# Kernel tuning notes

Measured on AMD Instinct MI355X. Metric: run time of the kernel, lower is better.

The kernel has to match this reference:

```python
import jax, jax.numpy as jnp
import numpy as np

N_PFAS, N_GW, N_SW = 20000, 100000, 20000
D_IN, D_OUT = 64, 128
E_PG, E_GP, E_SP, E_PS = 1600000, 1600000, 400000, 400000


def setup_inputs() -> dict:
    key = jax.random.key(0)
    ks = jax.random.split(key, 32)
    nrm = lambda k, shp, s=1.0: jax.random.normal(k, shp, jnp.float32) * s
    W = 0.05  # weight init scale
    inp = {
        # node features
        "x_pfas": nrm(ks[0], (N_PFAS, D_IN)),
        "x_gw": nrm(ks[1], (N_GW, D_IN)),
        "x_sw": nrm(ks[2], (N_SW, D_IN)),
        # edge indices per relation (src, dst)
        "ei_pg_src": jax.random.randint(ks[3], (E_PG,), 0, N_PFAS),
        "ei_pg_dst": jax.random.randint(ks[4], (E_PG,), 0, N_GW),
        "ei_gp_src": jax.random.randint(ks[5], (E_GP,), 0, N_GW),
        "ei_gp_dst": jax.random.randint(ks[6], (E_GP,), 0, N_PFAS),
        "ei_sp_src": jax.random.randint(ks[7], (E_SP,), 0, N_SW),
        "ei_sp_dst": jax.random.randint(ks[8], (E_SP,), 0, N_PFAS),
        "ei_ps_src": jax.random.randint(ks[9], (E_PS,), 0, N_PFAS),
        "ei_ps_dst": jax.random.randint(ks[10], (E_PS,), 0, N_SW),
        # SAGEConv params per relation: lin_l (neighbors, with bias), lin_r (root, no bias)
        "Wl_pg": nrm(ks[11], (D_IN, D_OUT), W), "Wr_pg": nrm(ks[12], (D_IN, D_OUT), W), "b_pg": jnp.zeros((D_OUT,), jnp.float32),
        "Wl_gp": nrm(ks[13], (D_IN, D_OUT), W), "Wr_gp": nrm(ks[14], (D_IN, D_OUT), W), "b_gp": jnp.zeros((D_OUT,), jnp.float32),
        "Wl_sp": nrm(ks[15], (D_IN, D_OUT), W), "Wr_sp": nrm(ks[16], (D_IN, D_OUT), W), "b_sp": jnp.zeros((D_OUT,), jnp.float32),
        "Wl_ps": nrm(ks[17], (D_IN, D_OUT), W), "Wr_ps": nrm(ks[18], (D_IN, D_OUT), W), "b_ps": jnp.zeros((D_OUT,), jnp.float32),
        # final linear head + PReLU
        "W_lin": nrm(ks[19], (D_OUT, 1), W), "b_lin": jnp.zeros((1,), jnp.float32),
        "alpha": jnp.full((1,), 0.25, jnp.float32),
    }
    return inp


def _sage(x_src, x_dst, src, dst, Wl, Wr, b, n_dst):
    # PyG SAGEConv: out = lin_l(mean_{j in N(i)} x_j) + lin_r(x_i)
    msg = x_src[src]                                   # [E, D_in] gather
    agg = jax.ops.segment_sum(msg, dst, num_segments=n_dst)        # [n_dst, D_in]
    cnt = jax.ops.segment_sum(jnp.ones(src.shape, x_src.dtype), dst, num_segments=n_dst)
    mean = agg / jnp.maximum(cnt, 1.0)[:, None]
    return mean @ Wl + x_dst @ Wr + b


def _prelu(y, a):
    return jnp.where(y > 0, y, a * y)


def reference(x_pfas, x_gw, x_sw, ei_pg_src, ei_pg_dst, ei_gp_src, ei_gp_dst,
              ei_sp_src, ei_sp_dst, ei_ps_src, ei_ps_dst,
              Wl_pg, Wr_pg, b_pg, Wl_gp, Wr_gp, b_gp, Wl_sp, Wr_sp, b_sp,
              Wl_ps, Wr_ps, b_ps, W_lin, b_lin, alpha):
    # HeteroConv with aggr='sum': pfas_sites receives from two relations (summed)
    h_gw = jax.nn.relu(_sage(x_pfas, x_gw, ei_pg_src, ei_pg_dst, Wl_pg, Wr_pg, b_pg, N_GW))
    h_pfas = jax.nn.relu(
        _sage(x_gw, x_pfas, ei_gp_src, ei_gp_dst, Wl_gp, Wr_gp, b_gp, N_PFAS)
        + _sage(x_sw, x_pfas, ei_sp_src, ei_sp_dst, Wl_sp, Wr_sp, b_sp, N_PFAS))
    h_sw = jax.nn.relu(_sage(x_pfas, x_sw, ei_ps_src, ei_ps_dst, Wl_ps, Wr_ps, b_ps, N_SW))
    out_gw = _prelu(h_gw @ W_lin + b_lin, alpha)   # [N_GW, 1]
    out_sw = _prelu(h_sw @ W_lin + b_lin, alpha)   # [N_SW, 1]
    return (h_pfas, out_gw, out_sw)
```

## Files before the change

kernel.cpp:

```cpp
#include <hip/hip_runtime.h>
#include <hip/hip_bf16.h>

#define N_PFAS 20000
#define N_GW   100000
#define N_SW   20000
#define N_SEG  160000
#define BASE_GW 0
#define BASE_GP 100000
#define BASE_SP 120000
#define BASE_PS 140000
#define NBIN 1250
#define NB_FILL 512
#define SORT_CAP 12288
#define N_XROW 140000

typedef __attribute__((ext_vector_type(8))) short short8;
typedef __attribute__((ext_vector_type(4))) float f32x4;
typedef __attribute__((ext_vector_type(2))) float f32x2;

__device__ __forceinline__ unsigned short f2bf(float f) {
    union { float f; unsigned int u; } v;
    v.f = f;
    unsigned int u = v.u;
    unsigned int r = (u + 0x7fffu + ((u >> 16) & 1u)) >> 16;
    return (unsigned short)r;
}
__device__ __forceinline__ float lo_bf(unsigned int v) {
    union { unsigned int u; float f; } w; w.u = v << 16; return w.f;
}
__device__ __forceinline__ float hi_bf(unsigned int v) {
    union { unsigned int u; float f; } w; w.u = v & 0xffff0000u; return w.f;
}

#if __has_builtin(__builtin_amdgcn_cvt_pk_f32_fp8) && __has_builtin(__builtin_amdgcn_cvt_pk_fp8_f32)
#define FP8_HW 1
__device__ __forceinline__ unsigned int enc_fp8x4(float4 v) {
    int r = __builtin_amdgcn_cvt_pk_fp8_f32(v.x, v.y, 0, false);
    r = __builtin_amdgcn_cvt_pk_fp8_f32(v.z, v.w, r, true);
    return (unsigned int)r;
}
__device__ __forceinline__ void dec_fp8x4v(unsigned int u, f32x2& lo, f32x2& hi) {
    lo = __builtin_amdgcn_cvt_pk_f32_fp8(u, false);
    hi = __builtin_amdgcn_cvt_pk_f32_fp8(u, true);
}
#else
__device__ __forceinline__ unsigned char enc1_e5m2(float f) {
    union { unsigned short u; _Float16 h; } cv;
    cv.h = (_Float16)f;
    unsigned int u = cv.u;
    unsigned int r = (u + 0x7Fu + ((u >> 8) & 1u)) >> 8;
    return (unsigned char)(r > 255u ? 255u : r);
}
__device__ __forceinline__ unsigned int enc_fp8x4(float4 v) {
    return (unsigned int)enc1_e5m2(v.x) | ((unsigned int)enc1_e5m2(v.y) << 8)
         | ((unsigned int)enc1_e5m2(v.z) << 16) | ((unsigned int)enc1_e5m2(v.w) << 24);
}
__device__ __forceinline__ float dec1_e5m2(unsigned int b) {
    union { unsigned short u; _Float16 h; } cv;
    cv.u = (unsigned short)(b << 8);
    return (float)cv.h;
}
__device__ __forceinline__ void dec_fp8x4v(unsigned int u, f32x2& lo, f32x2& hi) {
    lo.x = dec1_e5m2(u & 0xFF); lo.y = dec1_e5m2((u >> 8) & 0xFF);
    hi.x = dec1_e5m2((u >> 16) & 0xFF); hi.y = dec1_e5m2(u >> 24);
}
#endif

__device__ __forceinline__ void edge_lookup(int i,
    const int* __restrict__ s0, const int* __restrict__ d0, int E0,
    const int* __restrict__ s1, const int* __restrict__ d1, int E1,
    const int* __restrict__ s2, const int* __restrict__ d2, int E2,
    const int* __restrict__ s3, const int* __restrict__ d3,
    int& g, int& sv)
{
    if (i < E0)                { g = BASE_GW + d0[i];                 sv = s0[i]; }
    else if (i < E0 + E1)      { int j = i - E0;           g = BASE_GP + d1[j]; sv = s1[j]; }
    else if (i < E0 + E1 + E2) { int j = i - E0 - E1;      g = BASE_SP + d2[j]; sv = s2[j]; }
    else                       { int j = i - E0 - E1 - E2; g = BASE_PS + d3[j]; sv = s3[j]; }
}

__global__ void __launch_bounds__(1024)
count_cast(const int* __restrict__ d0, int E0, const int* __restrict__ d1, int E1,
           const int* __restrict__ d2, int E2, const int* __restrict__ d3, int E3,
           const float* __restrict__ xp, const float* __restrict__ xg,
           const float* __restrict__ xs, unsigned short* __restrict__ x16,
           unsigned int* __restrict__ x8, int* __restrict__ countMat)
{
    const int T0 = 20000 * 16, T1 = 120000 * 16, TT = N_XROW * 16;
    for (int i = blockIdx.x * 1024 + threadIdx.x; i < TT; i += NB_FILL * 1024) {
        float4 v;
        if (i < T0)      v = ((const float4*)xp)[i];
        else if (i < T1) v = ((const float4*)xg)[i - T0];
        else             v = ((const float4*)xs)[i - T1];
        ushort4 o;
        o.x = f2bf(v.x); o.y = f2bf(v.y); o.z = f2bf(v.z); o.w = f2bf(v.w);
        ((ushort4*)x16)[i] = o;
        if (x8) x8[i] = enc_fp8x4(v);
    }

    __shared__ int h[NBIN];
    for (int i = threadIdx.x; i < NBIN; i += 1024) h[i] = 0;
    __syncthreads();
    int total = E0 + E1 + E2 + E3;
    int CH = (total + NB_FILL - 1) / NB_FILL;
    int s = blockIdx.x * CH;
    int e = s + CH; if (e > total) e = total;
    for (int i0 = s + threadIdx.x * 4; i0 < e; i0 += 1024 * 4) {
        int gs[4];
        int m = e - i0; if (m > 4) m = 4;
        #pragma unroll
        for (int u = 0; u < 4; u++) {
            if (u < m) {
                int g, sv;
                edge_lookup(i0 + u, nullptr, d0, E0, nullptr, d1, E1,
                            nullptr, d2, E2, nullptr, d3, g, gs[u]);
                gs[u] = g;
            }
        }
        #pragma unroll
        for (int u = 0; u < 4; u++)
            if (u < m) atomicAdd(&h[gs[u] >> 7], 1);
    }
    __syncthreads();
    for (int i = threadIdx.x; i < NBIN; i += 1024)
        countMat[blockIdx.x * NBIN + i] = h[i];
}

__global__ void __launch_bounds__(1024)
scan_part(const int* __restrict__ countMat, int* __restrict__ next,
          int* __restrict__ partials, int n)
{
    __shared__ int lds[1024];
    int i = blockIdx.x * 1024 + threadIdx.x;
    int v = 0;
    if (i < n) {
        int b = i >> 9, k = i & 511;
        v = countMat[k * NBIN + b];
    }
    lds[threadIdx.x] = v;
    __syncthreads();
    #pragma unroll
    for (int off = 1; off < 1024; off <<= 1) {
        int t = (threadIdx.x >= off) ? lds[threadIdx.x - off] : 0;
        __syncthreads();
        lds[threadIdx.x] += t;
        __syncthreads();
    }
    if (i < n) next[i] = lds[threadIdx.x] - v;
    if (threadIdx.x == 1023) partials[blockIdx.x] = lds[1023];
}

__device__ __forceinline__ int partials_prefix(const int* __restrict__ partials,
                                               int idx, int lane)
{
    int s = 0;
    for (int j = lane; j < idx; j += 64) s += partials[j];
    #pragma unroll
    for (int m = 32; m; m >>= 1) s += __shfl_xor(s, m);
    return s;
}

__global__ void __launch_bounds__(1024)
fill_bin(const int* __restrict__ s0, const int* __restrict__ d0, int E0,
         const int* __restrict__ s1, const int* __restrict__ d1, int E1,
         const int* __restrict__ s2, const int* __restrict__ d2, int E2,
         const int* __restrict__ s3, const int* __restrict__ d3, int E3,
         const int* __restrict__ next, const int* __restrict__ partials,
         int* __restrict__ edge_binned)
{
    __shared__ int cur[NBIN];
    __shared__ int sp[1024];
    {
        int t = threadIdx.x;
        int v = (t < 625) ? partials[t] : 0;
        sp[t] = v;
        __syncthreads();
        #pragma unroll
        for (int off = 1; off < 1024; off <<= 1) {
            int x = (t >= off) ? sp[t - off] : 0;
            __syncthreads();
            sp[t] += x;
            __syncthreads();
        }
        sp[t] -= v;
    }
    __syncthreads();
    for (int i = threadIdx.x; i < NBIN; i += 1024)
        cur[i] = next[i * NB_FILL + blockIdx.x] + sp[i >> 1];
    __syncthreads();
    int total = E0 + E1 + E2 + E3;
    int CH = (total + NB_FILL - 1) / NB_FILL;
    int s = blockIdx.x * CH;
    int e = s + CH; if (e > total) e = total;
    for (int i0 = s + threadIdx.x * 4; i0 < e; i0 += 1024 * 4) {
        int g[4], sv[4];
        int m = e - i0; if (m > 4) m = 4;
        #pragma unroll
        for (int u = 0; u < 4; u++)
            if (u < m) edge_lookup(i0 + u, s0, d0, E0, s1, d1, E1,
                                   s2, d2, E2, s3, d3, g[u], sv[u]);
        #pragma unroll
        for (int u = 0; u < 4; u++) {
            if (u < m) {
                int slot = atomicAdd(&cur[g[u] >> 7], 1);
                edge_binned[slot] = sv[u] | ((g[u] & 127) << 20);
            }
        }
    }
}

__global__ void __launch_bounds__(1024)
sort_bin(const int* __restrict__ next, const int* __restrict__ partials,
         int* __restrict__ edge_binned,
         int2* __restrict__ nodeMeta, int E_total)
{
    __shared__ int stage[SORT_CAP];
    __shared__ int cnt[128], basep[128], cur[128];
    int lane = threadIdx.x & 63;
    int b = (int)((blockIdx.x + 781u) % NBIN);
    int pA = partials_prefix(partials, b >> 1, lane);
    int start = next[b * NB_FILL] + pA;
    int end;
    if (b == NBIN - 1) end = E_total;
    else {
        int pB = pA + ((b & 1) ? partials[b >> 1] : 0);
        end = next[(b + 1) * NB_FILL] + pB;
    }
    int n = end - start;
    if (n > SORT_CAP) n = SORT_CAP;

    for (int i = threadIdx.x; i < n; i += 1024) stage[i] = edge_binned[start + i];
    if (threadIdx.x < 128) cnt[threadIdx.x] = 0;
    __syncthreads();
    for (int i = threadIdx.x; i < n; i += 1024) atomicAdd(&cnt[stage[i] >> 20], 1);
    __syncthreads();
    if (threadIdx.x < 128) basep[threadIdx.x] = cnt[threadIdx.x];
    __syncthreads();
    #pragma unroll
    for (int off = 1; off < 128; off <<= 1) {
        int v = 0;
        if (threadIdx.x < 128 && threadIdx.x >= off) v = basep[threadIdx.x - off];
        __syncthreads();
        if (threadIdx.x < 128) basep[threadIdx.x] += v;
        __syncthreads();
    }
    if (threadIdx.x < 128) {
        int ex = basep[threadIdx.x] - cnt[threadIdx.x];
        cur[threadIdx.x] = ex;
        int g = (b << 7) + threadIdx.x;
        nodeMeta[g] = make_int2(start + ex, cnt[threadIdx.x]);
    }
    __syncthreads();
    for (int i = threadIdx.x; i < n; i += 1024) {
        int w = stage[i];
        int dl = w >> 20;
        int g = (b << 7) + dl;
        int rb = (g < BASE_GP) ? 0 : (g < BASE_SP) ? 20000
               : (g < BASE_PS) ? 120000 : 0;
        int slot = atomicAdd(&cur[dl], 1);
        edge_binned[start + slot] = (w & 0xFFFFF) + rb;
    }
}

__global__ void __launch_bounds__(256)
agg_node8(const unsigned int* __restrict__ x8,
          const int2* __restrict__ nodeMeta,
          const int* __restrict__ edge_src, unsigned short* __restrict__ meanAll)
{
    int wpair = (blockIdx.x * blockDim.x + threadIdx.x) >> 6;
    int lane = threadIdx.x & 63;
    if (wpair >= N_SEG / 2) return;
    int h = lane >> 5;
    int wlin = 2 * wpair + h;
    int wid = (wlin < 60000) ? (BASE_GP + wlin) : (wlin - 60000);
    int eq = (lane >> 3) & 3;
    int fc = lane & 7;
    int l32 = lane & 31;
    int2 meta = nodeMeta[wid];
    int start = meta.x, cnt = meta.y;
    f32x2 a01 = {0.f,0.f}, a23 = {0.f,0.f}, a45 = {0.f,0.f}, a67 = {0.f,0.f};
    int j = 0;
    for (; j + 32 <= cnt; j += 32) {
        int ev = edge_src[start + j + l32];
        #pragma unroll
        for (int t = 0; t < 8; t++) {
            int id = __shfl(ev, h * 32 + 4 * t + eq);
            uint2 v = *(const uint2*)(x8 + (((size_t)id) << 4) + fc * 2);
            f32x2 lo0, hi0, lo1, hi1;
            dec_fp8x4v(v.x, lo0, hi0);
            dec_fp8x4v(v.y, lo1, hi1);
            a01 += lo0; a23 += hi0; a45 += lo1; a67 += hi1;
        }
    }
    if (j < cnt) {
        int blk = cnt - j;
        int ev = (l32 < blk) ? edge_src[start + j + l32] : 0;
        int ng = (blk + 3) >> 2;
        for (int t = 0; t < ng; t++) {
            int idx = 4 * t + eq;
            int id = __shfl(ev, h * 32 + idx);
            if (idx < blk) {
                uint2 v = *(const uint2*)(x8 + (((size_t)id) << 4) + fc * 2);
                f32x2 lo0, hi0, lo1, hi1;
                dec_fp8x4v(v.x, lo0, hi0);
                dec_fp8x4v(v.y, lo1, hi1);
                a01 += lo0; a23 += hi0; a45 += lo1; a67 += hi1;
            }
        }
    }
    float f[8] = {a01.x, a01.y, a23.x, a23.y, a45.x, a45.y, a67.x, a67.y};
    #pragma unroll
    for (int r = 0; r < 8; r++) {
        f[r] += __shfl_xor(f[r], 8);
        f[r] += __shfl_xor(f[r], 16);
    }
    if (eq == 0) {
        float inv = 1.0f / (float)(cnt > 1 ? cnt : 1);
        ushort4 o0, o1;
        o0.x = f2bf(f[0] * inv); o0.y = f2bf(f[1] * inv);
        o0.z = f2bf(f[2] * inv); o0.w = f2bf(f[3] * inv);
        o1.x = f2bf(f[4] * inv); o1.y = f2bf(f[5] * inv);
        o1.z = f2bf(f[6] * inv); o1.w = f2bf(f[7] * inv);
        ushort4* dst = (ushort4*)(meanAll + (size_t)wid * 64 + fc * 8);
        dst[0] = o0;
        dst[1] = o1;
    }
}

__global__ void __launch_bounds__(256)
agg_node16(const unsigned short* __restrict__ x16,
           const int2* __restrict__ nodeMeta,
           const int* __restrict__ edge_src, unsigned short* __restrict__ meanAll)
{
    int wlin = (blockIdx.x * blockDim.x + threadIdx.x) >> 6;
    int lane = threadIdx.x & 63;
    if (wlin >= N_SEG) return;
    int wid = (wlin < 60000) ? (BASE_GP + wlin) : (wlin - 60000);
    int quarter = lane >> 4;
    int fcol = lane & 15;
    int2 meta = nodeMeta[wid];
    int start = meta.x, cnt = meta.y;
    float a0 = 0.f, a1 = 0.f, a2 = 0.f, a3 = 0.f;
    int j = 0;
    while (j + 64 <= cnt) {
        int ev = edge_src[start + j + lane];
        #pragma unroll
        for (int t = 0; t < 16; t++) {
            int id = __shfl(ev, 4 * t + quarter);
            uint2 v = ((const uint2*)(x16 + (((size_t)id) << 6)))[fcol];
            a0 += lo_bf(v.x); a1 += hi_bf(v.x);
            a2 += lo_bf(v.y); a3 += hi_bf(v.y);
        }
        j += 64;
    }
    if (j < cnt) {
        int blk = cnt - j;
        int ev = (lane < blk) ? edge_src[start + j + lane] : 0;
        int ng = (blk + 3) >> 2;
        #pragma unroll 4
        for (int t = 0; t < ng; t++) {
            int idx = 4 * t + quarter;
            int id = __shfl(ev, idx);
            if (idx < blk) {
                uint2 v = ((const uint2*)(x16 + (((size_t)id) << 6)))[fcol];
                a0 += lo_bf(v.x); a1 += hi_bf(v.x);
                a2 += lo_bf(v.y); a3 += hi_bf(v.y);
            }
        }
    }
    a0 += __shfl_xor(a0, 16); a1 += __shfl_xor(a1, 16);
    a2 += __shfl_xor(a2, 16); a3 += __shfl_xor(a3, 16);
    a0 += __shfl_xor(a0, 32); a1 += __shfl_xor(a1, 32);
    a2 += __shfl_xor(a2, 32); a3 += __shfl_xor(a3, 32);
    if (quarter == 0) {
        float inv = 1.0f / (float)(cnt > 1 ? cnt : 1);
        ushort4 o;
        o.x = f2bf(a0 * inv); o.y = f2bf(a1 * inv);
        o.z = f2bf(a2 * inv); o.w = f2bf(a3 * inv);
        ((ushort4*)meanAll)[(size_t)wid * 16 + fcol] = o;
    }
}

__device__ __forceinline__ void
head_body(const unsigned short* __restrict__ x16r,
          const unsigned short* __restrict__ mean,
          const float* __restrict__ Wl, const float* __restrict__ Wr,
          const float* __restrict__ b, const float* __restrict__ Wlin,
          const float* __restrict__ b_lin, const float* __restrict__ alpha,
          float* __restrict__ out, int N, int bid, int nblocks,
          unsigned short* __restrict__ smem)
{
    unsigned short* sW = smem;

    for (int i = threadIdx.x; i < 64 * 128; i += 256) {
        int k = i >> 7, col = i & 127;
        sW[col * 136 + k]      = f2bf(Wl[k * 128 + col]);
        sW[col * 136 + 64 + k] = f2bf(Wr[k * 128 + col]);
    }

    int lane = threadIdx.x & 63;
    int wid  = threadIdx.x >> 6;
    int c    = lane & 15;
    int quad = lane >> 4;
    float wl_c[8], b_c[8];
    #pragma unroll
    for (int t = 0; t < 8; t++) {
        wl_c[t] = Wlin[t * 16 + c];
        b_c[t]  = b[t * 16 + c];
    }
    float blin = b_lin[0], al = alpha[0];
    __syncthreads();

    int ntiles = (N + 63) >> 6;
    for (int tile = bid; tile < ntiles; tile += nblocks) {
        int base = tile << 6;
        int node = base + wid * 16 + c;
        bool valid = node < N;
        const unsigned short* mrow = mean + (size_t)node * 64;
        const unsigned short* xrow = x16r + (size_t)node * 64;

        f32x4 acc[8] = {};
        #pragma unroll
        for (int step = 0; step < 4; step++) {
            short8 a = {};
            if (valid) {
                const unsigned short* src = (step < 2)
                    ? (mrow + step * 32 + quad * 8)
                    : (xrow + (step - 2) * 32 + quad * 8);
                a = *(const short8*)src;
            }
            #pragma unroll
            for (int t = 0; t < 8; t++) {
                short8 bb = *(const short8*)&sW[(t * 16 + c) * 136 + step * 32 + quad * 8];
                acc[t] = __builtin_amdgcn_mfma_f32_16x16x32_bf16(a, bb, acc[t], 0, 0, 0);
            }
        }

        float p[4] = {0.f, 0.f, 0.f, 0.f};
        #pragma unroll
        for (int t = 0; t < 8; t++) {
            #pragma unroll
            for (int r = 0; r < 4; r++) {
                float h = fmaxf(acc[t][r] + b_c[t], 0.0f);
                p[r] += h * wl_c[t];
            }
        }
        #pragma unroll
        for (int m = 1; m < 16; m <<= 1) {
            #pragma unroll
            for (int r = 0; r < 4; r++) p[r] += __shfl_xor(p[r], m);
        }
        if (c == 0) {
            #pragma unroll
            for (int r = 0; r < 4; r++) {
                int onode = base + wid * 16 + quad * 4 + r;
                if (onode < N) {
                    float y = p[r] + blin;
                    out[onode] = y > 0.0f ? y : al * y;
                }
            }
        }
    }
}

__device__ __forceinline__ void
pfas_body(const unsigned short* __restrict__ x16p,
          const unsigned short* __restrict__ meanGP,
          const unsigned short* __restrict__ meanSP,
          const float* __restrict__ WlGP, const float* __restrict__ WrGP,
          const float* __restrict__ bGP,
          const float* __restrict__ WlSP, const float* __restrict__ WrSP,
          const float* __restrict__ bSP,
          float* __restrict__ out, int N, int bid, int nblocks,
          unsigned short* __restrict__ smem)
{
    unsigned short* sW = smem;

    for (int i = threadIdx.x; i < 64 * 128; i += 256) {
        int k = i >> 7, col = i & 127;
        sW[col * 200 + k]       = f2bf(WlGP[k * 128 + col]);
        sW[col * 200 + 64 + k]  = f2bf(WlSP[k * 128 + col]);
        sW[col * 200 + 128 + k] = f2bf(WrGP[k * 128 + col] + WrSP[k * 128 + col]);
    }

    int lane = threadIdx.x & 63;
    int wid  = threadIdx.x >> 6;
    int c    = lane & 15;
    int quad = lane >> 4;
    int rg   = (wid & 1) * 16;
    int cg   = (wid >> 1) * 4;
    float b_c[4];
    #pragma unroll
    for (int t = 0; t < 4; t++)
        b_c[t] = bGP[(cg + t) * 16 + c] + bSP[(cg + t) * 16 + c];
    __syncthreads();

    int ntiles = (N + 31) >> 5;
    for (int tile = bid; tile < ntiles; tile += nblocks) {
        int base = tile << 5;
        int node = base + rg + c;
        bool valid = node < N;
        const unsigned short* grow = meanGP + (size_t)node * 64;
        const unsigned short* srow = meanSP + (size_t)node * 64;
        const unsigned short* xrow = x16p + (size_t)node * 64;

        f32x4 acc[4] = {};
        #pragma unroll
        for (int step = 0; step < 6; step++) {
            short8 a = {};
            if (valid) {
                const unsigned short* src = (step < 2)
                    ? (grow + step * 32 + quad * 8)
                    : (step < 4) ? (srow + (step - 2) * 32 + quad * 8)
                                 : (xrow + (step - 4) * 32 + quad * 8);
                a = *(const short8*)src;
            }
            #pragma unroll
            for (int t = 0; t < 4; t++) {
                short8 bb = *(const short8*)&sW[((cg + t) * 16 + c) * 200 + step * 32 + quad * 8];
                acc[t] = __builtin_amdgcn_mfma_f32_16x16x32_bf16(a, bb, acc[t], 0, 0, 0);
            }
        }

        #pragma unroll
        for (int t = 0; t < 4; t++) {
            int col = (cg + t) * 16 + c;
            #pragma unroll
            for (int r = 0; r < 4; r++) {
                int onode = base + rg + quad * 4 + r;
                if (onode < N) {
                    float h = fmaxf(acc[t][r] + b_c[t], 0.0f);
                    out[(size_t)onode * 128 + col] = h;
                }
            }
        }
    }
}

__global__ void __launch_bounds__(256)
node_mfma(const unsigned short* __restrict__ x16,
          const unsigned short* __restrict__ meanAll,
          const float* __restrict__ Wl_pg, const float* __restrict__ Wr_pg,
          const float* __restrict__ b_pg,
          const float* __restrict__ Wl_ps, const float* __restrict__ Wr_ps,
          const float* __restrict__ b_ps,
          const float* __restrict__ Wl_gp, const float* __restrict__ Wr_gp,
          const float* __restrict__ b_gp,
          const float* __restrict__ Wl_sp, const float* __restrict__ Wr_sp,
          const float* __restrict__ b_sp,
          const float* __restrict__ W_lin, const float* __restrict__ b_lin,
          const float* __restrict__ alpha,
          float* __restrict__ out_gw, float* __restrict__ out_sw,
          float* __restrict__ out_pfas)
{
    __shared__ __align__(16) unsigned short smem[25600];
    int bx = blockIdx.x;
    if (bx < 512) {
        head_body(x16 + (size_t)20000 * 64, meanAll + (size_t)BASE_GW * 64,
                  Wl_pg, Wr_pg, b_pg, W_lin, b_lin, alpha,
                  out_gw, N_GW, bx, 512, smem);
    } else if (bx < 672) {
        head_body(x16 + (size_t)120000 * 64, meanAll + (size_t)BASE_PS * 64,
                  Wl_ps, Wr_ps, b_ps, W_lin, b_lin, alpha,
                  out_sw, N_SW, bx - 512, 160, smem);
    } else {
        pfas_body(x16, meanAll + (size_t)BASE_GP * 64, meanAll + (size_t)BASE_SP * 64,
                  Wl_gp, Wr_gp, b_gp, Wl_sp, Wr_sp, b_sp,
                  out_pfas, N_PFAS, bx - 672, 224, smem);
    }
}

extern "C" void kernel_launch(void* const* d_in, const int* in_sizes, int n_in,
                              void* d_out, int out_size, void* d_ws, size_t ws_size,
                              hipStream_t stream)
{
    const float* x_pfas = (const float*)d_in[0];
    const float* x_gw   = (const float*)d_in[1];
    const float* x_sw   = (const float*)d_in[2];
    const int* pg_src = (const int*)d_in[3];
    const int* pg_dst = (const int*)d_in[4];
    const int* gp_src = (const int*)d_in[5];
    const int* gp_dst = (const int*)d_in[6];
    const int* sp_src = (const int*)d_in[7];
    const int* sp_dst = (const int*)d_in[8];
    const int* ps_src = (const int*)d_in[9];
    const int* ps_dst = (const int*)d_in[10];
    const float* Wl_pg = (const float*)d_in[11];
    const float* Wr_pg = (const float*)d_in[12];
    const float* b_pg  = (const float*)d_in[13];
    const float* Wl_gp = (const float*)d_in[14];
    const float* Wr_gp = (const float*)d_in[15];
    const float* b_gp  = (const float*)d_in[16];
    const float* Wl_sp = (const float*)d_in[17];
    const float* Wr_sp = (const float*)d_in[18];
    const float* b_sp  = (const float*)d_in[19];
    const float* Wl_ps = (const float*)d_in[20];
    const float* Wr_ps = (const float*)d_in[21];
    const float* b_ps  = (const float*)d_in[22];
    const float* W_lin = (const float*)d_in[23];
    const float* b_lin = (const float*)d_in[24];
    const float* alpha = (const float*)d_in[25];

    float* out = (float*)d_out;
    float* out_pfas = out;
    float* out_gw   = out + (size_t)N_PFAS * 128;
    float* out_sw   = out_gw + N_GW;

    int E_PG = in_sizes[3];
    int E_GP = in_sizes[5];
    int E_SP = in_sizes[7];
    int E_PS = in_sizes[9];
    int E_total = E_PG + E_GP + E_SP + E_PS;

    unsigned short* meanAll = (unsigned short*)d_ws;
    int* countMat  = (int*)(meanAll + (size_t)N_SEG * 64);
    int2* nodeMeta = (int2*)countMat;
    int* next      = countMat + NB_FILL * NBIN;
    int* partials  = next + NB_FILL * NBIN;
    int* edge_binned = partials + 1024;
    unsigned short* x16 = (unsigned short*)(edge_binned + E_total);
    unsigned int* x8 = (unsigned int*)(x16 + (size_t)N_XROW * 64);
    size_t needed8 = (size_t)((char*)(x8 + (size_t)N_XROW * 16) - (char*)d_ws);
    bool use8 = (ws_size >= needed8);

    const int SCAN_N  = NB_FILL * NBIN;
    const int SCAN_NB = SCAN_N / 1024;

    count_cast<<<NB_FILL, 1024, 0, stream>>>(pg_dst, E_PG, gp_dst, E_GP,
                                             sp_dst, E_SP, ps_dst, E_PS,
                                             x_pfas, x_gw, x_sw, x16,
                                             use8 ? x8 : (unsigned int*)nullptr,
                                             countMat);

    scan_part<<<SCAN_NB, 1024, 0, stream>>>(countMat, next, partials, SCAN_N);

    fill_bin<<<NB_FILL, 1024, 0, stream>>>(pg_src, pg_dst, E_PG,
                                           gp_src, gp_dst, E_GP,
                                           sp_src, sp_dst, E_SP,
                                           ps_src, ps_dst, E_PS,
                                           next, partials, edge_binned);

    sort_bin<<<NBIN, 1024, 0, stream>>>(next, partials, edge_binned,
                                        nodeMeta, E_total);

    if (use8) {
        agg_node8<<<(N_SEG / 2 * 64 + 255) / 256, 256, 0, stream>>>(x8, nodeMeta,
                                                                    edge_binned, meanAll);
    } else {
        agg_node16<<<(N_SEG * 64 + 255) / 256, 256, 0, stream>>>(x16, nodeMeta,
                                                                 edge_binned, meanAll);
    }

    node_mfma<<<896, 256, 0, stream>>>(x16, meanAll,
                                       Wl_pg, Wr_pg, b_pg,
                                       Wl_ps, Wr_ps, b_ps,
                                       Wl_gp, Wr_gp, b_gp,
                                       Wl_sp, Wr_sp, b_sp,
                                       W_lin, b_lin, alpha,
                                       out_gw, out_sw, out_pfas);
}
```

Baseline: 295.8 us.

## Fuse per-bin counting sort with fp8 neighbor aggregation into one kernel

Replaces the separate sort_bin and agg_node8 kernels on the fp8 path with a single sort_agg kernel. Each block sorts its bin's edges into shared memory and then aggregates the 128 destination nodes directly from LDS. This removes the write-back and re-read of sorted edges and nodeMeta through global memory, and one kernel launch. In exchange, gather parallelism is limited to 1250 blocks of 1024 threads, each wave handling 4 nodes in sequence, and the high LDS use per block may lower occupancy.

Result: faster. 286.2 us (-3.2%).

```diff
diff --git a/kernel.cpp b/kernel.cpp
--- a/kernel.cpp
+++ b/kernel.cpp
@@ -113,7 +113,7 @@
             if (u < m) {
                 int g, sv;
                 edge_lookup(i0 + u, nullptr, d0, E0, nullptr, d1, E1,
-                            nullptr, d2, E2, nullptr, d3, g, gs[u]);
+                            nullptr, d2, E2, nullptr, d3, g, sv);
                 gs[u] = g;
             }
         }
@@ -205,6 +205,124 @@
                 int slot = atomicAdd(&cur[g[u] >> 7], 1);
                 edge_binned[slot] = sv[u] | ((g[u] & 127) << 20);
             }
+        }
+    }
+}
+
+__global__ void __launch_bounds__(1024)
+sort_agg(const int* __restrict__ next, const int* __restrict__ partials,
+         const int* __restrict__ edge_binned,
+         const unsigned int* __restrict__ x8,
+         unsigned short* __restrict__ meanAll, int E_total)
+{
+    __shared__ int stage[SORT_CAP];
+    __shared__ int cnt[128], basep[128], cur[128], lstart[128];
+    int lane = threadIdx.x & 63;
+    int b = (int)((blockIdx.x + 781u) % NBIN);
+    int pA = partials_prefix(partials, b >> 1, lane);
+    int start = next[b * NB_FILL] + pA;
+    int end;
+    if (b == NBIN - 1) end = E_total;
+    else {
+        int pB = pA + ((b & 1) ? partials[b >> 1] : 0);
+        end = next[(b + 1) * NB_FILL] + pB;
+    }
+    int n = end - start;
+    if (n > SORT_CAP) n = SORT_CAP;
+
+    int vals[12];
+    int nv = 0;
+    if (threadIdx.x < 128) cnt[threadIdx.x] = 0;
+    __syncthreads();
+    for (int i = threadIdx.x; i < n; i += 1024) {
+        int w = edge_binned[start + i];
+        vals[nv++] = w;
+        atomicAdd(&cnt[w >> 20], 1);
+    }
+    __syncthreads();
+    if (threadIdx.x < 128) basep[threadIdx.x] = cnt[threadIdx.x];
+    __syncthreads();
+    #pragma unroll
+    for (int off = 1; off < 128; off <<= 1) {
+        int v = 0;
+        if (threadIdx.x < 128 && threadIdx.x >= off) v = basep[threadIdx.x - off];
+        __syncthreads();
+        if (threadIdx.x < 128) basep[threadIdx.x] += v;
+        __syncthreads();
+    }
+    if (threadIdx.x < 128) {
+        int ex = basep[threadIdx.x] - cnt[threadIdx.x];
+        cur[threadIdx.x] = ex;
+        lstart[threadIdx.x] = ex;
+    }
+    __syncthreads();
+    for (int u = 0; u < nv; u++) {
+        int w = vals[u];
+        int dl = w >> 20;
+        int g = (b << 7) + dl;
+        int rb = (g < BASE_GP) ? 0 : (g < BASE_SP) ? 20000
+               : (g < BASE_PS) ? 120000 : 0;
+        int slot = atomicAdd(&cur[dl], 1);
+        stage[slot] = (w & 0xFFFFF) + rb;
+    }
+    __syncthreads();
+
+    int wv = threadIdx.x >> 6;
+    int h  = lane >> 5;
+    int eq = (lane >> 3) & 3;
+    int fc = lane & 7;
+    int l32 = lane & 31;
+    for (int it = 0; it < 4; it++) {
+        int nl = 2 * (it * 16 + wv) + h;
+        int s0 = lstart[nl];
+        int c0 = cnt[nl];
+        f32x2 a01 = {0.f,0.f}, a23 = {0.f,0.f}, a45 = {0.f,0.f}, a67 = {0.f,0.f};
+        int j = 0;
+        for (; j + 32 <= c0; j += 32) {
+            int ev = stage[s0 + j + l32];
+            #pragma unroll
+            for (int t = 0; t < 8; t++) {
+                int id = __shfl(ev, h * 32 + 4 * t + eq);
+                uint2 v = *(const uint2*)(x8 + (((size_t)id) << 4) + fc * 2);
+                f32x2 lo0, hi0, lo1, hi1;
+                dec_fp8x4v(v.x, lo0, hi0);
+                dec_fp8x4v(v.y, lo1, hi1);
+                a01 += lo0; a23 += hi0; a45 += lo1; a67 += hi1;
+            }
+        }
+        if (j < c0) {
+            int blk = c0 - j;
+            int ev = (l32 < blk) ? stage[s0 + j + l32] : 0;
+            int ng = (blk + 3) >> 2;
+            for (int t = 0; t < ng; t++) {
+                int idx = 4 * t + eq;
+                int id = __shfl(ev, h * 32 + idx);
+                if (idx < blk) {
+                    uint2 v = *(const uint2*)(x8 + (((size_t)id) << 4) + fc * 2);
+                    f32x2 lo0, hi0, lo1, hi1;
+                    dec_fp8x4v(v.x, lo0, hi0);
+                    dec_fp8x4v(v.y, lo1, hi1);
+                    a01 += lo0; a23 += hi0; a45 += lo1; a67 += hi1;
+                }
+            }
+        }
+        float f[8] = {a01.x, a01.y, a23.x, a23.y, a45.x, a45.y, a67.x, a67.y};
+        #pragma unroll
+        for (int r = 0; r < 8; r++) {
+            f[r] += __shfl_xor(f[r], 8);
+            f[r] += __shfl_xor(f[r], 16);
+        }
+        if (eq == 0) {
+            float inv = 1.0f / (float)(c0 > 1 ? c0 : 1);
+            ushort4 o0, o1;
+            o0.x = f2bf(f[0] * inv); o0.y = f2bf(f[1] * inv);
+            o0.z = f2bf(f[2] * inv); o0.w = f2bf(f[3] * inv);
+            o1.x = f2bf(f[4] * inv); o1.y = f2bf(f[5] * inv);
+            o1.z = f2bf(f[6] * inv); o1.w = f2bf(f[7] * inv);
+            int gnode = (b << 7) + nl;
+            ushort4* dst = (ushort4*)(meanAll + (size_t)gnode * 64 + fc * 8);
+            dst[0] = o0;
+            dst[1] = o1;
         }
     }
 }
@@ -259,71 +377,6 @@
                : (g < BASE_PS) ? 120000 : 0;
         int slot = atomicAdd(&cur[dl], 1);
         edge_binned[start + slot] = (w & 0xFFFFF) + rb;
-    }
-}
-
-__global__ void __launch_bounds__(256)
-agg_node8(const unsigned int* __restrict__ x8,
-          const int2* __restrict__ nodeMeta,
-          const int* __restrict__ edge_src, unsigned short* __restrict__ meanAll)
-{
-    int wpair = (blockIdx.x * blockDim.x + threadIdx.x) >> 6;
-    int lane = threadIdx.x & 63;
-    if (wpair >= N_SEG / 2) return;
-    int h = lane >> 5;
-    int wlin = 2 * wpair + h;
-    int wid = (wlin < 60000) ? (BASE_GP + wlin) : (wlin - 60000);
-    int eq = (lane >> 3) & 3;
-    int fc = lane & 7;
-    int l32 = lane & 31;
-    int2 meta = nodeMeta[wid];
-    int start = meta.x, cnt = meta.y;
-    f32x2 a01 = {0.f,0.f}, a23 = {0.f,0.f}, a45 = {0.f,0.f}, a67 = {0.f,0.f};
-    int j = 0;
-    for (; j + 32 <= cnt; j += 32) {
-        int ev = edge_src[start + j + l32];
-        #pragma unroll
-        for (int t = 0; t < 8; t++) {
-            int id = __shfl(ev, h * 32 + 4 * t + eq);
-            uint2 v = *(const uint2*)(x8 + (((size_t)id) << 4) + fc * 2);
-            f32x2 lo0, hi0, lo1, hi1;
-            dec_fp8x4v(v.x, lo0, hi0);
-            dec_fp8x4v(v.y, lo1, hi1);
-            a01 += lo0; a23 += hi0; a45 += lo1; a67 += hi1;
-        }
-    }
-    if (j < cnt) {
-        int blk = cnt - j;
-        int ev = (l32 < blk) ? edge_src[start + j + l32] : 0;
-        int ng = (blk + 3) >> 2;
-        for (int t = 0; t < ng; t++) {
-            int idx = 4 * t + eq;
-            int id = __shfl(ev, h * 32 + idx);
-            if (idx < blk) {
-                uint2 v = *(const uint2*)(x8 + (((size_t)id) << 4) + fc * 2);
-                f32x2 lo0, hi0, lo1, hi1;
-                dec_fp8x4v(v.x, lo0, hi0);
-                dec_fp8x4v(v.y, lo1, hi1);
-                a01 += lo0; a23 += hi0; a45 += lo1; a67 += hi1;
-            }
-        }
-    }
-    float f[8] = {a01.x, a01.y, a23.x, a23.y, a45.x, a45.y, a67.x, a67.y};
-    #pragma unroll
-    for (int r = 0; r < 8; r++) {
-        f[r] += __shfl_xor(f[r], 8);
-        f[r] += __shfl_xor(f[r], 16);
-    }
-    if (eq == 0) {
-        float inv = 1.0f / (float)(cnt > 1 ? cnt : 1);
-        ushort4 o0, o1;
-        o0.x = f2bf(f[0] * inv); o0.y = f2bf(f[1] * inv);
-        o0.z = f2bf(f[2] * inv); o0.w = f2bf(f[3] * inv);
-        o1.x = f2bf(f[4] * inv); o1.y = f2bf(f[5] * inv);
-        o1.z = f2bf(f[6] * inv); o1.w = f2bf(f[7] * inv);
-        ushort4* dst = (ushort4*)(meanAll + (size_t)wid * 64 + fc * 8);
-        dst[0] = o0;
-        dst[1] = o1;
     }
 }
 
@@ -640,13 +693,12 @@
                                            ps_src, ps_dst, E_PS,
                                            next, partials, edge_binned);
 
-    sort_bin<<<NBIN, 1024, 0, stream>>>(next, partials, edge_binned,
-                                        nodeMeta, E_total);
-
     if (use8) {
-        agg_node8<<<(N_SEG / 2 * 64 + 255) / 256, 256, 0, stream>>>(x8, nodeMeta,
-                                                                    edge_binned, meanAll);
+        sort_agg<<<NBIN, 1024, 0, stream>>>(next, partials, edge_binned,
+                                            x8, meanAll, E_total);
     } else {
+        sort_bin<<<NBIN, 1024, 0, stream>>>(next, partials, edge_binned,
+                                            nodeMeta, E_total);
         agg_node16<<<(N_SEG * 64 + 255) / 256, 256, 0, stream>>>(x16, nodeMeta,
                                                                  edge_binned, meanAll);
     }
```
